# Performance work log

Hardware: AMD Instinct MI355X
Metric: run time of the kernel (lower is better)

Reference implementation:

```python
import jax, jax.numpy as jnp
import numpy as np

NUM_EXPERTS = 8
HIDDEN = 2048
FFN = 1376
CAPACITY_FACTOR = 1.25
SCORE_SCALE = 1.0


def setup_inputs() -> dict:
    key = jax.random.key(0)
    k = jax.random.split(key, 6)
    T = 8192
    x = jax.random.normal(k[0], (T, HIDDEN), dtype=jnp.float32)
    topK_indices = jax.random.randint(k[1], (T,), 0, NUM_EXPERTS, dtype=jnp.int64)
    topK_scores = jax.random.uniform(k[2], (T,), dtype=jnp.float32)
    s = 1.0 / np.sqrt(HIDDEN)
    w_gate = jax.random.normal(k[3], (NUM_EXPERTS, HIDDEN, FFN), dtype=jnp.float32) * s
    w_up = jax.random.normal(k[4], (NUM_EXPERTS, HIDDEN, FFN), dtype=jnp.float32) * s
    w_down = jax.random.normal(k[5], (NUM_EXPERTS, FFN, HIDDEN), dtype=jnp.float32) * (1.0 / np.sqrt(FFN))
    return {"x": x, "topK_indices": topK_indices, "topK_scores": topK_scores,
            "w_gate": w_gate, "w_up": w_up, "w_down": w_down}


def reference(x, topK_indices, topK_scores, w_gate, w_up, w_down):
    T, D = x.shape
    E = w_gate.shape[0]
    capacity = int(CAPACITY_FACTOR * T / E)  # static (depends only on shapes)
    # position of each token within its assigned expert (deterministic drop:
    # keep the first `capacity` tokens in sequence order per expert)
    oh = jax.nn.one_hot(topK_indices, E, dtype=jnp.int32)          # [T,E]
    rank = jnp.take_along_axis(jnp.cumsum(oh, axis=0) - 1,
                               topK_indices[:, None].astype(jnp.int32), axis=1)[:, 0]
    keep = rank < capacity                                          # [T]
    # dispatch into per-expert capacity buffers; dropped tokens go to dummy slot
    slot = jnp.where(keep, topK_indices.astype(jnp.int32) * capacity + rank, E * capacity)
    buf = jnp.zeros((E * capacity + 1, D), x.dtype)
    buf = buf.at[slot].set(jnp.where(keep[:, None], x, jnp.zeros_like(x)))
    xe = buf[:E * capacity].reshape(E, capacity, D)                 # [E,C,D]
    # per-expert SwiGLU MLP as grouped GEMMs
    h = jax.nn.silu(jnp.einsum('ecd,edf->ecf', xe, w_gate)) * jnp.einsum('ecd,edf->ecf', xe, w_up)
    out = jnp.einsum('ecf,efd->ecd', h, w_down).reshape(E * capacity, D)
    out = jnp.concatenate([out, jnp.zeros((1, D), out.dtype)], axis=0)
    # combine: dropped tokens -> zero (dropped_padding='zero'), gate-score fusion
    y = out[slot] * keep[:, None].astype(out.dtype)
    y = y * (topK_scores[:, None] * SCORE_SCALE)
    return y
```

## Files before the change

kernel.cpp:

```cpp
#include <hip/hip_runtime.h>
#include <hip/hip_bf16.h>
#include <cstdint>
#include <cstddef>

#define NTOK 8192
#define DH   2048
#define DF   1376
#define NE   8
#define CAP  1280

typedef __bf16 bf16x8 __attribute__((ext_vector_type(8)));
typedef float  f32x4  __attribute__((ext_vector_type(4)));

#define BARRIER() asm volatile("s_barrier" ::: "memory")
#define WAITV(n)  asm volatile("s_waitcnt vmcnt(" #n ")" ::: "memory")
#define LGKM0()   asm volatile("s_waitcnt lgkmcnt(0)" ::: "memory")
#define SCHED0()  __builtin_amdgcn_sched_barrier(0)
#define SETPRIO(n) __builtin_amdgcn_s_setprio(n)

__device__ __forceinline__ uint32_t pk2(float a, float b) {
  float2 f; f.x = a; f.y = b;
  union { __hip_bfloat162 h; uint32_t u; } cv;
  cv.h = __float22bfloat162_rn(f);
  return cv.u;
}
__device__ __forceinline__ ushort bf16bits(float a) {
  return (ushort)(pk2(a, 0.f) & 0xFFFFu);
}
__device__ __forceinline__ void gload16(const ushort* g, ushort* l) {
  __builtin_amdgcn_global_load_lds(
      (const __attribute__((address_space(1))) uint32_t*)(const void*)g,
      (__attribute__((address_space(3))) uint32_t*)(void*)l,
      16, 0, 0);
}

__device__ __forceinline__ void rp_src(int o, int& row, int& ko) {
  int p = o >> 7;
  int g = ((o >> 4) & 7) ^ (p & 7);
  row = p * 2 + (g >> 2);
  ko  = (g & 3) * 8;
}
__device__ __forceinline__ int rp_off(int row, int l4) {
  return ((row >> 1) << 7) + (((((row & 1) << 2) + l4) ^ ((row >> 1) & 7)) << 4);
}

__global__ void routing_kernel(const int* __restrict__ idx, int* __restrict__ tok_slot,
                               int* __restrict__ tok_keep) {
  __shared__ int cnt[256][NE];
  const int t = threadIdx.x;
  for (int s = t; s < NE * CAP; s += 256) tok_slot[s] = -1;
  unsigned long long cA = 0ull, cB = 0ull;
  const int per = NTOK / 256, base = t * per;
  for (int i = 0; i < per; ++i) {
    int e = idx[base + i];
    unsigned long long inc = 1ull << ((e & 3) * 16);
    if (e < 4) cA += inc; else cB += inc;
  }
#pragma unroll
  for (int e = 0; e < 4; ++e) cnt[t][e]     = (int)((cA >> (e * 16)) & 0xFFFF);
#pragma unroll
  for (int e = 0; e < 4; ++e) cnt[t][4 + e] = (int)((cB >> (e * 16)) & 0xFFFF);
  __syncthreads();
  if (t < NE) {
    int run = 0;
    for (int i = 0; i < 256; ++i) { int c = cnt[i][t]; cnt[i][t] = run; run += c; }
  }
  __syncthreads();
  cA = 0ull; cB = 0ull;
#pragma unroll
  for (int e = 0; e < 4; ++e) cA |= (unsigned long long)(cnt[t][e] & 0xFFFF) << (e * 16);
#pragma unroll
  for (int e = 0; e < 4; ++e) cB |= (unsigned long long)(cnt[t][4 + e] & 0xFFFF) << (e * 16);
  for (int i = 0; i < per; ++i) {
    int token = base + i;
    int e = idx[token];
    int sh = (e & 3) * 16;
    int r = (int)(((e < 4 ? cA : cB) >> sh) & 0xFFFF);
    unsigned long long inc = 1ull << sh;
    if (e < 4) cA += inc; else cB += inc;
    bool keep = (r < CAP);
    tok_keep[token] = keep ? 1 : 0;
    if (keep) tok_slot[e * CAP + r] = token;
  }
}

__global__ void xconv_zero(const float* __restrict__ x, const int* __restrict__ keep,
                           ushort* __restrict__ xb, float* __restrict__ y) {
  const int row = blockIdx.x;
  const int c = threadIdx.x * 8;
  const size_t off = (size_t)row * DH + c;
  float4 a = *(const float4*)(x + off);
  float4 b = *(const float4*)(x + off + 4);
  uint4 p = { pk2(a.x, a.y), pk2(a.z, a.w), pk2(b.x, b.y), pk2(b.z, b.w) };
  *(uint4*)(xb + off) = p;
  if (!keep[row]) {
    float4 z = {0.f, 0.f, 0.f, 0.f};
    *(float4*)(y + off) = z;
    *(float4*)(y + off + 4) = z;
  }
}

__global__ __launch_bounds__(256) void transpose_all(
    const float* __restrict__ wg, const float* __restrict__ wu, const float* __restrict__ wd,
    ushort* __restrict__ wgt, ushort* __restrict__ wut, ushort* __restrict__ wdt) {
  const int z = blockIdx.z;
  const float* in; ushort* out; int K, N, eidx;
  if (z < 8)       { in = wg; out = wgt; K = DH; N = DF; eidx = z; }
  else if (z < 16) { in = wu; out = wut; K = DH; N = DF; eidx = z - 8; }
  else             { in = wd; out = wdt; K = DF; N = DH; eidx = z - 16; }
  const int n0 = blockIdx.x * 64, k0 = blockIdx.y * 64;
  if (n0 >= N || k0 >= K) return;
  __shared__ ushort T[64][72];
  const int tid = threadIdx.x;
  const size_t eoff_in  = (size_t)eidx * K * N;
  const size_t eoff_out = (size_t)eidx * N * K;
  const int kr = tid >> 4;
  const int nc = (tid & 15) * 4;
#pragma unroll
  for (int it = 0; it < 4; ++it) {
    int k = k0 + kr + it * 16;
    int n = n0 + nc;
    float4 v = {0.f, 0.f, 0.f, 0.f};
    if (k < K && n + 4 <= N) v = *(const float4*)(in + eoff_in + (size_t)k * N + n);
    T[nc + 0][kr + it * 16] = bf16bits(v.x);
    T[nc + 1][kr + it * 16] = bf16bits(v.y);
    T[nc + 2][kr + it * 16] = bf16bits(v.z);
    T[nc + 3][kr + it * 16] = bf16bits(v.w);
  }
  __syncthreads();
  const int nr = tid >> 2;
  const int kc = tid & 3;
#pragma unroll
  for (int it = 0; it < 2; ++it) {
    int kloc = kc * 16 + it * 8;
    int n = n0 + nr, k = k0 + kloc;
    if (n < N && k + 8 <= K)
      *(uint4*)(out + eoff_out + (size_t)n * K + k) = *(const uint4*)&T[nr][kloc];
  }
}

__global__ __launch_bounds__(512, 4) void gemm_gateup4(
    const ushort* __restrict__ xb, const ushort* __restrict__ wgt,
    const ushort* __restrict__ wut, const int* __restrict__ tok_slot,
    ushort* __restrict__ h)
{
  __shared__ __align__(16) char sm[73728];
  const int tid = threadIdx.x, lane = tid & 63, wid = tid >> 6;
  const int wr = wid >> 1, wc = wid & 1;
  const int l15 = lane & 15, l4 = lane >> 4;

  int wgid = (blockIdx.x & 7) * 110 + (blockIdx.x >> 3);
  const int e = wgid / 110;
  const int rem = wgid - e * 110;
  const int mt = rem % 10, nt = rem / 10;
  const int n0 = nt * 128;

  const ushort* srcA; const ushort* srcBg; const ushort* srcBu;
  {
    int o = wid * 1024 + lane * 16;
    int row, ko; rp_src(o, row, ko);
    int tk = tok_slot[e * CAP + mt * 128 + row];
    if (tk < 0) tk = 0;
    srcA = xb + (size_t)tk * DH + ko;
    int n = n0 + row; if (n > DF - 1) n = DF - 1;
    srcBg = wgt + ((size_t)e * DF + n) * DH + ko;
    srcBu = wut + ((size_t)e * DF + n) * DH + ko;
  }
  int aoff[2], boff[4];
#pragma unroll
  for (int i = 0; i < 2; ++i) aoff[i] = rp_off(wr * 32 + i * 16 + l15, l4);
#pragma unroll
  for (int j = 0; j < 4; ++j) boff[j] = rp_off(wc * 64 + j * 16 + l15, l4);
  const int dstw = wid * 1024;

  f32x4 accG[2][4], accU[2][4];
#pragma unroll
  for (int i = 0; i < 2; ++i)
#pragma unroll
    for (int j = 0; j < 4; ++j) {
      accG[i][j] = (f32x4){0.f, 0.f, 0.f, 0.f};
      accU[i][j] = (f32x4){0.f, 0.f, 0.f, 0.f};
    }

  const int NT = DH / 32;
#pragma unroll
  for (int t0 = 0; t0 < 2; ++t0) {
    int kk = t0 * 32;
    gload16(srcA  + kk, (ushort*)(sm + t0 * 8192 + dstw));
    gload16(srcBg + kk, (ushort*)(sm + 24576 + t0 * 8192 + dstw));
    gload16(srcBu + kk, (ushort*)(sm + 49152 + t0 * 8192 + dstw));
  }
  WAITV(3);
  BARRIER();

  int rb = 0, wb = 2;
  for (int t = 0; t < NT; ++t) {
    char* Ab  = sm + rb * 8192;
    char* Bgb = sm + 24576 + rb * 8192;
    char* Bub = sm + 49152 + rb * 8192;
    if (t + 2 < NT) {
      const int kk = (t + 2) * 32;
      gload16(srcA  + kk, (ushort*)(sm + wb * 8192 + dstw));
      gload16(srcBg + kk, (ushort*)(sm + 24576 + wb * 8192 + dstw));
      gload16(srcBu + kk, (ushort*)(sm + 49152 + wb * 8192 + dstw));
    }
    bf16x8 a[2], b[4];
#pragma unroll
    for (int i = 0; i < 2; ++i) a[i] = *(const bf16x8*)(Ab + aoff[i]);
#pragma unroll
    for (int j = 0; j < 4; ++j) b[j] = *(const bf16x8*)(Bgb + boff[j]);
    LGKM0(); SCHED0();
    SETPRIO(1);
#pragma unroll
    for (int j = 0; j < 4; ++j)
#pragma unroll
      for (int i = 0; i < 2; ++i)
        accG[i][j] = __builtin_amdgcn_mfma_f32_16x16x32_bf16(a[i], b[j], accG[i][j], 0, 0, 0);
    SETPRIO(0); SCHED0();
#pragma unroll
    for (int j = 0; j < 4; ++j) b[j] = *(const bf16x8*)(Bub + boff[j]);
    LGKM0(); SCHED0();
    SETPRIO(1);
#pragma unroll
    for (int j = 0; j < 4; ++j)
#pragma unroll
      for (int i = 0; i < 2; ++i)
        accU[i][j] = __builtin_amdgcn_mfma_f32_16x16x32_bf16(a[i], b[j], accU[i][j], 0, 0, 0);
    SETPRIO(0); SCHED0();
    if (t + 2 < NT) { WAITV(3); } else { WAITV(0); }
    BARRIER();
    rb = (rb == 2) ? 0 : rb + 1;
    wb = (wb == 2) ? 0 : wb + 1;
  }
  const size_t rowbase = (size_t)(e * CAP + mt * 128 + wr * 32);
#pragma unroll
  for (int j = 0; j < 4; ++j) {
    int col = n0 + wc * 64 + j * 16 + l15;
    if (col < DF) {
#pragma unroll
      for (int i = 0; i < 2; ++i)
#pragma unroll
        for (int r2 = 0; r2 < 4; ++r2) {
          size_t row = rowbase + i * 16 + l4 * 4 + r2;
          float gv = accG[i][j][r2], uv = accU[i][j][r2];
          h[row * DF + col] = bf16bits(gv / (1.f + __expf(-gv)) * uv);
        }
    }
  }
}

__global__ __launch_bounds__(512, 4) void gemm_down4(
    const ushort* __restrict__ h, const ushort* __restrict__ wdt,
    const int* __restrict__ tok_slot, const float* __restrict__ scores,
    float* __restrict__ y)
{
  __shared__ __align__(16) char sm[50176];
  int* tokc = (int*)(sm + 49152);
  float* scc = (float*)(sm + 49664);
  const int tid = threadIdx.x, lane = tid & 63, wid = tid >> 6;
  const int wr = wid >> 1, wc = wid & 1;
  const int l15 = lane & 15, l4 = lane >> 4;

  int wgid = (blockIdx.x & 7) * 160 + (blockIdx.x >> 3);
  const int e = wgid / 160;
  const int rem = wgid - e * 160;
  const int mt = rem % 10, nt = rem / 10;
  const int n0 = nt * 128;

  if (tid < 128) {
    int tk = tok_slot[e * CAP + mt * 128 + tid];
    tokc[tid] = tk;
    scc[tid] = (tk >= 0) ? scores[tk] : 0.f;
  }
  __syncthreads();

  const size_t hrow0 = (size_t)(e * CAP + mt * 128);
  const ushort* srcA; const ushort* srcB;
  {
    int o = wid * 1024 + lane * 16;
    int row, ko; rp_src(o, row, ko);
    srcA = h + (hrow0 + row) * DF + ko;
    srcB = wdt + ((size_t)e * DH + n0 + row) * DF + ko;
  }
  int aoff[2], boff[4];
#pragma unroll
  for (int i = 0; i < 2; ++i) aoff[i] = rp_off(wr * 32 + i * 16 + l15, l4);
#pragma unroll
  for (int j = 0; j < 4; ++j) boff[j] = rp_off(wc * 64 + j * 16 + l15, l4);
  const int dstw = wid * 1024;

  f32x4 acc[2][4];
#pragma unroll
  for (int i = 0; i < 2; ++i)
#pragma unroll
    for (int j = 0; j < 4; ++j) acc[i][j] = (f32x4){0.f, 0.f, 0.f, 0.f};

  const int NT = DF / 32;
#pragma unroll
  for (int t0 = 0; t0 < 2; ++t0) {
    int kk = t0 * 32;
    gload16(srcA + kk, (ushort*)(sm + t0 * 8192 + dstw));
    gload16(srcB + kk, (ushort*)(sm + 24576 + t0 * 8192 + dstw));
  }
  WAITV(2);
  BARRIER();

  int rb = 0, wb = 2;
  for (int t = 0; t < NT; ++t) {
    char* Ab = sm + rb * 8192;
    char* Bb = sm + 24576 + rb * 8192;
    if (t + 2 < NT) {
      const int kk = (t + 2) * 32;
      gload16(srcA + kk, (ushort*)(sm + wb * 8192 + dstw));
      gload16(srcB + kk, (ushort*)(sm + 24576 + wb * 8192 + dstw));
    }
    bf16x8 a[2], b[4];
#pragma unroll
    for (int i = 0; i < 2; ++i) a[i] = *(const bf16x8*)(Ab + aoff[i]);
#pragma unroll
    for (int j = 0; j < 4; ++j) b[j] = *(const bf16x8*)(Bb + boff[j]);
    LGKM0(); SCHED0();
    SETPRIO(1);
#pragma unroll
    for (int j = 0; j < 4; ++j)
#pragma unroll
      for (int i = 0; i < 2; ++i)
        acc[i][j] = __builtin_amdgcn_mfma_f32_16x16x32_bf16(a[i], b[j], acc[i][j], 0, 0, 0);
    SETPRIO(0); SCHED0();
    if (t + 2 < NT) { WAITV(2); } else { WAITV(0); }
    BARRIER();
    rb = (rb == 2) ? 0 : rb + 1;
    wb = (wb == 2) ? 0 : wb + 1;
  }
  int tkr[2][4]; float sr[2][4];
#pragma unroll
  for (int i = 0; i < 2; ++i)
#pragma unroll
    for (int r = 0; r < 4; ++r) {
      int rl = wr * 32 + i * 16 + l4 * 4 + r;
      tkr[i][r] = tokc[rl];
      sr[i][r]  = scc[rl];
    }
#pragma unroll
  for (int j = 0; j < 4; ++j) {
    int col = n0 + wc * 64 + j * 16 + l15;
#pragma unroll
    for (int i = 0; i < 2; ++i)
#pragma unroll
      for (int r = 0; r < 4; ++r)
        if (tkr[i][r] >= 0)
          y[(size_t)tkr[i][r] * DH + col] = acc[i][j][r] * sr[i][r];
  }
}

extern "C" void kernel_launch(void* const* d_in, const int* in_sizes, int n_in,
                              void* d_out, int out_size, void* d_ws, size_t ws_size,
                              hipStream_t stream) {
  const float* x   = (const float*)d_in[0];
  const int*   idx = (const int*)d_in[1];
  const float* sc  = (const float*)d_in[2];
  const float* wg  = (const float*)d_in[3];
  const float* wu  = (const float*)d_in[4];
  const float* wd  = (const float*)d_in[5];
  float* y = (float*)d_out;

  const size_t OFF_KEEP = 40960;
  const size_t OFF_H    = 73728;
  const size_t SZ_H     = (size_t)NE * CAP * DF * 2;
  const size_t OFF_XB   = OFF_H + SZ_H;
  const size_t SZ_XB    = (size_t)NTOK * DH * 2;
  const size_t OFF_WGT  = OFF_XB + SZ_XB;
  const size_t SZ_W     = (size_t)NE * DH * DF * 2;
  const size_t OFF_WUT  = OFF_WGT + SZ_W;
  const size_t OFF_WDT  = OFF_WUT + SZ_W;

  int* tok_slot = (int*)d_ws;
  int* tok_keep = (int*)((char*)d_ws + OFF_KEEP);
  ushort* hbuf = (ushort*)((char*)d_ws + OFF_H);
  ushort* xb   = (ushort*)((char*)d_ws + OFF_XB);
  ushort* wgt  = (ushort*)((char*)d_ws + OFF_WGT);
  ushort* wut  = (ushort*)((char*)d_ws + OFF_WUT);
  ushort* wdt  = (ushort*)((char*)d_ws + OFF_WDT);

  hipLaunchKernelGGL(routing_kernel, dim3(1), dim3(256), 0, stream, idx, tok_slot, tok_keep);
  hipLaunchKernelGGL(xconv_zero, dim3(NTOK), dim3(256), 0, stream, x, tok_keep, xb, y);
  hipLaunchKernelGGL(transpose_all, dim3(32, 32, 24), dim3(256), 0, stream,
                     wg, wu, wd, wgt, wut, wdt);
  hipLaunchKernelGGL(gemm_gateup4, dim3(880), dim3(512), 0, stream,
                     xb, wgt, wut, tok_slot, hbuf);
  hipLaunchKernelGGL(gemm_down4, dim3(1280), dim3(512), 0, stream,
                     hbuf, wdt, tok_slot, sc, y);
}
```

Baseline: 347.1 us.

## Make grouped GEMM kernels persistent with atomic tile counter scheduling

Both expert GEMM kernels become persistent: a fixed grid of 512 workgroups repeatedly claims tile indices from a global atomic counter until all tiles are done. The routing kernel zeroes the two counters. The aim is to remove wave-quantization tail effects and per-block launch overhead by matching the grid to resident capacity. In exchange it adds a per-tile atomic and barrier, and it drops the earlier XCD-aware mapping of blocks to experts, which may reduce L2 locality for the weights.

Result: slower. 388.5 us (+11.9%).

```diff
diff --git a/kernel.cpp b/kernel.cpp
--- a/kernel.cpp
+++ b/kernel.cpp
@@ -9,6 +9,9 @@
 #define NE   8
 #define CAP  1280
 
+#define GU_NTILES 880
+#define DN_NTILES 1280
+
 typedef __bf16 bf16x8 __attribute__((ext_vector_type(8)));
 typedef float  f32x4  __attribute__((ext_vector_type(4)));
 
@@ -45,9 +48,10 @@
 }
 
 __global__ void routing_kernel(const int* __restrict__ idx, int* __restrict__ tok_slot,
-                               int* __restrict__ tok_keep) {
+                               int* __restrict__ tok_keep, int* __restrict__ ctrs) {
   __shared__ int cnt[256][NE];
   const int t = threadIdx.x;
+  if (t < 2) ctrs[t] = 0;
   for (int s = t; s < NE * CAP; s += 256) tok_slot[s] = -1;
   unsigned long long cA = 0ull, cB = 0ull;
   const int per = NTOK / 256, base = t * per;
@@ -139,33 +143,17 @@
   }
 }
 
-__global__ __launch_bounds__(512, 4) void gemm_gateup4(
+__global__ __launch_bounds__(512, 4) void gemm_gateup6(
     const ushort* __restrict__ xb, const ushort* __restrict__ wgt,
     const ushort* __restrict__ wut, const int* __restrict__ tok_slot,
-    ushort* __restrict__ h)
+    ushort* __restrict__ h, int* __restrict__ ctr)
 {
   __shared__ __align__(16) char sm[73728];
+  __shared__ int tile_s;
   const int tid = threadIdx.x, lane = tid & 63, wid = tid >> 6;
   const int wr = wid >> 1, wc = wid & 1;
   const int l15 = lane & 15, l4 = lane >> 4;
 
-  int wgid = (blockIdx.x & 7) * 110 + (blockIdx.x >> 3);
-  const int e = wgid / 110;
-  const int rem = wgid - e * 110;
-  const int mt = rem % 10, nt = rem / 10;
-  const int n0 = nt * 128;
-
-  const ushort* srcA; const ushort* srcBg; const ushort* srcBu;
-  {
-    int o = wid * 1024 + lane * 16;
-    int row, ko; rp_src(o, row, ko);
-    int tk = tok_slot[e * CAP + mt * 128 + row];
-    if (tk < 0) tk = 0;
-    srcA = xb + (size_t)tk * DH + ko;
-    int n = n0 + row; if (n > DF - 1) n = DF - 1;
-    srcBg = wgt + ((size_t)e * DF + n) * DH + ko;
-    srcBu = wut + ((size_t)e * DF + n) * DH + ko;
-  }
   int aoff[2], boff[4];
 #pragma unroll
   for (int i = 0; i < 2; ++i) aoff[i] = rp_off(wr * 32 + i * 16 + l15, l4);
@@ -173,115 +161,119 @@
   for (int j = 0; j < 4; ++j) boff[j] = rp_off(wc * 64 + j * 16 + l15, l4);
   const int dstw = wid * 1024;
 
-  f32x4 accG[2][4], accU[2][4];
-#pragma unroll
-  for (int i = 0; i < 2; ++i)
+  int srow, sko;
+  { int o = wid * 1024 + lane * 16; rp_src(o, srow, sko); }
+
+  for (;;) {
+    if (tid == 0) tile_s = atomicAdd(ctr, 1);
+    __syncthreads();
+    const int tile = tile_s;
+    if (tile >= GU_NTILES) break;
+    const int e = tile / 110;
+    const int rem = tile - e * 110;
+    const int nt = rem / 10, mt = rem - (rem / 10) * 10;
+    const int n0 = nt * 128;
+
+    const ushort* srcA; const ushort* srcBg; const ushort* srcBu;
+    {
+      int tk = tok_slot[e * CAP + mt * 128 + srow];
+      if (tk < 0) tk = 0;
+      srcA = xb + (size_t)tk * DH + sko;
+      int n = n0 + srow; if (n > DF - 1) n = DF - 1;
+      srcBg = wgt + ((size_t)e * DF + n) * DH + sko;
+      srcBu = wut + ((size_t)e * DF + n) * DH + sko;
+    }
+
+    f32x4 accG[2][4], accU[2][4];
+#pragma unroll
+    for (int i = 0; i < 2; ++i)
+#pragma unroll
+      for (int j = 0; j < 4; ++j) {
+        accG[i][j] = (f32x4){0.f, 0.f, 0.f, 0.f};
+        accU[i][j] = (f32x4){0.f, 0.f, 0.f, 0.f};
+      }
+
+    const int NT = DH / 32;
+#pragma unroll
+    for (int t0 = 0; t0 < 2; ++t0) {
+      int kk = t0 * 32;
+      gload16(srcA  + kk, (ushort*)(sm + t0 * 8192 + dstw));
+      gload16(srcBg + kk, (ushort*)(sm + 24576 + t0 * 8192 + dstw));
+      gload16(srcBu + kk, (ushort*)(sm + 49152 + t0 * 8192 + dstw));
+    }
+    WAITV(3);
+    BARRIER();
+
+    int rb = 0, wb = 2;
+    for (int t = 0; t < NT; ++t) {
+      char* Ab  = sm + rb * 8192;
+      char* Bgb = sm + 24576 + rb * 8192;
+      char* Bub = sm + 49152 + rb * 8192;
+      if (t + 2 < NT) {
+        const int kk = (t + 2) * 32;
+        gload16(srcA  + kk, (ushort*)(sm + wb * 8192 + dstw));
+        gload16(srcBg + kk, (ushort*)(sm + 24576 + wb * 8192 + dstw));
+        gload16(srcBu + kk, (ushort*)(sm + 49152 + wb * 8192 + dstw));
+      }
+      bf16x8 a[2], b[4];
+#pragma unroll
+      for (int i = 0; i < 2; ++i) a[i] = *(const bf16x8*)(Ab + aoff[i]);
+#pragma unroll
+      for (int j = 0; j < 4; ++j) b[j] = *(const bf16x8*)(Bgb + boff[j]);
+      LGKM0(); SCHED0();
+      SETPRIO(1);
+#pragma unroll
+      for (int j = 0; j < 4; ++j)
+#pragma unroll
+        for (int i = 0; i < 2; ++i)
+          accG[i][j] = __builtin_amdgcn_mfma_f32_16x16x32_bf16(a[i], b[j], accG[i][j], 0, 0, 0);
+      SETPRIO(0); SCHED0();
+#pragma unroll
+      for (int j = 0; j < 4; ++j) b[j] = *(const bf16x8*)(Bub + boff[j]);
+      LGKM0(); SCHED0();
+      SETPRIO(1);
+#pragma unroll
+      for (int j = 0; j < 4; ++j)
+#pragma unroll
+        for (int i = 0; i < 2; ++i)
+          accU[i][j] = __builtin_amdgcn_mfma_f32_16x16x32_bf16(a[i], b[j], accU[i][j], 0, 0, 0);
+      SETPRIO(0); SCHED0();
+      if (t + 2 < NT) { WAITV(3); } else { WAITV(0); }
+      BARRIER();
+      rb = (rb == 2) ? 0 : rb + 1;
+      wb = (wb == 2) ? 0 : wb + 1;
+    }
+    const size_t rowbase = (size_t)(e * CAP + mt * 128 + wr * 32);
 #pragma unroll
     for (int j = 0; j < 4; ++j) {
-      accG[i][j] = (f32x4){0.f, 0.f, 0.f, 0.f};
-      accU[i][j] = (f32x4){0.f, 0.f, 0.f, 0.f};
-    }
-
-  const int NT = DH / 32;
-#pragma unroll
-  for (int t0 = 0; t0 < 2; ++t0) {
-    int kk = t0 * 32;
-    gload16(srcA  + kk, (ushort*)(sm + t0 * 8192 + dstw));
-    gload16(srcBg + kk, (ushort*)(sm + 24576 + t0 * 8192 + dstw));
-    gload16(srcBu + kk, (ushort*)(sm + 49152 + t0 * 8192 + dstw));
-  }
-  WAITV(3);
-  BARRIER();
-
-  int rb = 0, wb = 2;
-  for (int t = 0; t < NT; ++t) {
-    char* Ab  = sm + rb * 8192;
-    char* Bgb = sm + 24576 + rb * 8192;
-    char* Bub = sm + 49152 + rb * 8192;
-    if (t + 2 < NT) {
-      const int kk = (t + 2) * 32;
-      gload16(srcA  + kk, (ushort*)(sm + wb * 8192 + dstw));
-      gload16(srcBg + kk, (ushort*)(sm + 24576 + wb * 8192 + dstw));
-      gload16(srcBu + kk, (ushort*)(sm + 49152 + wb * 8192 + dstw));
-    }
-    bf16x8 a[2], b[4];
-#pragma unroll
-    for (int i = 0; i < 2; ++i) a[i] = *(const bf16x8*)(Ab + aoff[i]);
-#pragma unroll
-    for (int j = 0; j < 4; ++j) b[j] = *(const bf16x8*)(Bgb + boff[j]);
-    LGKM0(); SCHED0();
-    SETPRIO(1);
-#pragma unroll
-    for (int j = 0; j < 4; ++j)
-#pragma unroll
-      for (int i = 0; i < 2; ++i)
-        accG[i][j] = __builtin_amdgcn_mfma_f32_16x16x32_bf16(a[i], b[j], accG[i][j], 0, 0, 0);
-    SETPRIO(0); SCHED0();
-#pragma unroll
-    for (int j = 0; j < 4; ++j) b[j] = *(const bf16x8*)(Bub + boff[j]);
-    LGKM0(); SCHED0();
-    SETPRIO(1);
-#pragma unroll
-    for (int j = 0; j < 4; ++j)
-#pragma unroll
-      for (int i = 0; i < 2; ++i)
-        accU[i][j] = __builtin_amdgcn_mfma_f32_16x16x32_bf16(a[i], b[j], accU[i][j], 0, 0, 0);
-    SETPRIO(0); SCHED0();
-    if (t + 2 < NT) { WAITV(3); } else { WAITV(0); }
-    BARRIER();
-    rb = (rb == 2) ? 0 : rb + 1;
-    wb = (wb == 2) ? 0 : wb + 1;
-  }
-  const size_t rowbase = (size_t)(e * CAP + mt * 128 + wr * 32);
-#pragma unroll
-  for (int j = 0; j < 4; ++j) {
-    int col = n0 + wc * 64 + j * 16 + l15;
-    if (col < DF) {
-#pragma unroll
-      for (int i = 0; i < 2; ++i)
-#pragma unroll
-        for (int r2 = 0; r2 < 4; ++r2) {
-          size_t row = rowbase + i * 16 + l4 * 4 + r2;
-          float gv = accG[i][j][r2], uv = accU[i][j][r2];
-          h[row * DF + col] = bf16bits(gv / (1.f + __expf(-gv)) * uv);
-        }
-    }
-  }
-}
-
-__global__ __launch_bounds__(512, 4) void gemm_down4(
+      int col = n0 + wc * 64 + j * 16 + l15;
+      if (col < DF) {
+#pragma unroll
+        for (int i = 0; i < 2; ++i)
+#pragma unroll
+          for (int r2 = 0; r2 < 4; ++r2) {
+            size_t row = rowbase + i * 16 + l4 * 4 + r2;
+            float gv = accG[i][j][r2], uv = accU[i][j][r2];
+            h[row * DF + col] = bf16bits(gv / (1.f + __expf(-gv)) * uv);
+          }
+      }
+    }
+  }
+}
+
+__global__ __launch_bounds__(512, 4) void gemm_down6(
     const ushort* __restrict__ h, const ushort* __restrict__ wdt,
     const int* __restrict__ tok_slot, const float* __restrict__ scores,
-    float* __restrict__ y)
+    float* __restrict__ y, int* __restrict__ ctr)
 {
   __shared__ __align__(16) char sm[50176];
+  __shared__ int tile_s;
   int* tokc = (int*)(sm + 49152);
   float* scc = (float*)(sm + 49664);
   const int tid = threadIdx.x, lane = tid & 63, wid = tid >> 6;
   const int wr = wid >> 1, wc = wid & 1;
   const int l15 = lane & 15, l4 = lane >> 4;
 
-  int wgid = (blockIdx.x & 7) * 160 + (blockIdx.x >> 3);
-  const int e = wgid / 160;
-  const int rem = wgid - e * 160;
-  const int mt = rem % 10, nt = rem / 10;
-  const int n0 = nt * 128;
-
-  if (tid < 128) {
-    int tk = tok_slot[e * CAP + mt * 128 + tid];
-    tokc[tid] = tk;
-    scc[tid] = (tk >= 0) ? scores[tk] : 0.f;
-  }
-  __syncthreads();
-
-  const size_t hrow0 = (size_t)(e * CAP + mt * 128);
-  const ushort* srcA; const ushort* srcB;
-  {
-    int o = wid * 1024 + lane * 16;
-    int row, ko; rp_src(o, row, ko);
-    srcA = h + (hrow0 + row) * DF + ko;
-    srcB = wdt + ((size_t)e * DH + n0 + row) * DF + ko;
-  }
   int aoff[2], boff[4];
 #pragma unroll
   for (int i = 0; i < 2; ++i) aoff[i] = rp_off(wr * 32 + i * 16 + l15, l4);
@@ -289,67 +281,86 @@
   for (int j = 0; j < 4; ++j) boff[j] = rp_off(wc * 64 + j * 16 + l15, l4);
   const int dstw = wid * 1024;
 
-  f32x4 acc[2][4];
-#pragma unroll
-  for (int i = 0; i < 2; ++i)
-#pragma unroll
-    for (int j = 0; j < 4; ++j) acc[i][j] = (f32x4){0.f, 0.f, 0.f, 0.f};
-
-  const int NT = DF / 32;
-#pragma unroll
-  for (int t0 = 0; t0 < 2; ++t0) {
-    int kk = t0 * 32;
-    gload16(srcA + kk, (ushort*)(sm + t0 * 8192 + dstw));
-    gload16(srcB + kk, (ushort*)(sm + 24576 + t0 * 8192 + dstw));
-  }
-  WAITV(2);
-  BARRIER();
-
-  int rb = 0, wb = 2;
-  for (int t = 0; t < NT; ++t) {
-    char* Ab = sm + rb * 8192;
-    char* Bb = sm + 24576 + rb * 8192;
-    if (t + 2 < NT) {
-      const int kk = (t + 2) * 32;
-      gload16(srcA + kk, (ushort*)(sm + wb * 8192 + dstw));
-      gload16(srcB + kk, (ushort*)(sm + 24576 + wb * 8192 + dstw));
-    }
-    bf16x8 a[2], b[4];
-#pragma unroll
-    for (int i = 0; i < 2; ++i) a[i] = *(const bf16x8*)(Ab + aoff[i]);
-#pragma unroll
-    for (int j = 0; j < 4; ++j) b[j] = *(const bf16x8*)(Bb + boff[j]);
-    LGKM0(); SCHED0();
-    SETPRIO(1);
-#pragma unroll
-    for (int j = 0; j < 4; ++j)
+  int srow, sko;
+  { int o = wid * 1024 + lane * 16; rp_src(o, srow, sko); }
+
+  for (;;) {
+    if (tid == 0) tile_s = atomicAdd(ctr, 1);
+    __syncthreads();
+    const int tile = tile_s;
+    if (tile >= DN_NTILES) break;
+    const int e = tile / 160;
+    const int rem = tile - e * 160;
+    const int nt = rem / 10, mt = rem - (rem / 10) * 10;
+    const int n0 = nt * 128;
+
+    if (tid < 128) {
+      int tk = tok_slot[e * CAP + mt * 128 + tid];
+      tokc[tid] = tk;
+      scc[tid] = (tk >= 0) ? scores[tk] : 0.f;
+    }
+    __syncthreads();
+
+    const size_t hrow0 = (size_t)(e * CAP + mt * 128);
+    const ushort* srcA = h + (hrow0 + srow) * DF + sko;
+    const ushort* srcB = wdt + ((size_t)e * DH + n0 + srow) * DF + sko;
+
+    f32x4 acc[2][4];
+#pragma unroll
+    for (int i = 0; i < 2; ++i)
+#pragma unroll
+      for (int j = 0; j < 4; ++j) acc[i][j] = (f32x4){0.f, 0.f, 0.f, 0.f};
+
+    const int NT = DF / 32;
+#pragma unroll
+    for (int t0 = 0; t0 < 2; ++t0) {
+      int kk = t0 * 32;
+      gload16(srcA + kk, (ushort*)(sm + t0 * 8192 + dstw));
+      gload16(srcB + kk, (ushort*)(sm + 24576 + t0 * 8192 + dstw));
+    }
+    WAITV(2);
+    BARRIER();
+
+    int rb = 0, wb = 2;
+    for (int t = 0; t < NT; ++t) {
+      char* Ab = sm + rb * 8192;
+      char* Bb = sm + 24576 + rb * 8192;
+      if (t + 2 < NT) {
+        const int kk = (t + 2) * 32;
+        gload16(srcA + kk, (ushort*)(sm + wb * 8192 + dstw));
+        gload16(srcB + kk, (ushort*)(sm + 24576 + wb * 8192 + dstw));
+      }
+      bf16x8 a[2], b[4];
+#pragma unroll
+      for (int i = 0; i < 2; ++i) a[i] = *(const bf16x8*)(Ab + aoff[i]);
+#pragma unroll
+      for (int j = 0; j < 4; ++j) b[j] = *(const bf16x8*)(Bb + boff[j]);
+      LGKM0(); SCHED0();
+      SETPRIO(1);
+#pragma unroll
+      for (int j = 0; j < 4; ++j)
+#pragma unroll
+        for (int i = 0; i < 2; ++i)
+          acc[i][j] = __builtin_amdgcn_mfma_f32_16x16x32_bf16(a[i], b[j], acc[i][j], 0, 0, 0);
+      SETPRIO(0); SCHED0();
+      if (t + 2 < NT) { WAITV(2); } else { WAITV(0); }
+      BARRIER();
+      rb = (rb == 2) ? 0 : rb + 1;
+      wb = (wb == 2) ? 0 : wb + 1;
+    }
+#pragma unroll
+    for (int j = 0; j < 4; ++j) {
+      int col = n0 + wc * 64 + j * 16 + l15;
 #pragma unroll
       for (int i = 0; i < 2; ++i)
-        acc[i][j] = __builtin_amdgcn_mfma_f32_16x16x32_bf16(a[i], b[j], acc[i][j], 0, 0, 0);
-    SETPRIO(0); SCHED0();
-    if (t + 2 < NT) { WAITV(2); } else { WAITV(0); }
-    BARRIER();
-    rb = (rb == 2) ? 0 : rb + 1;
-    wb = (wb == 2) ? 0 : wb + 1;
-  }
-  int tkr[2][4]; float sr[2][4];
-#pragma unroll
-  for (int i = 0; i < 2; ++i)
-#pragma unroll
-    for (int r = 0; r < 4; ++r) {
-      int rl = wr * 32 + i * 16 + l4 * 4 + r;
-      tkr[i][r] = tokc[rl];
-      sr[i][r]  = scc[rl];
-    }
-#pragma unroll
-  for (int j = 0; j < 4; ++j) {
-    int col = n0 + wc * 64 + j * 16 + l15;
-#pragma unroll
-    for (int i = 0; i < 2; ++i)
-#pragma unroll
-      for (int r = 0; r < 4; ++r)
-        if (tkr[i][r] >= 0)
-          y[(size_t)tkr[i][r] * DH + col] = acc[i][j][r] * sr[i][r];
+#pragma unroll
+        for (int r = 0; r < 4; ++r) {
+          int rl = wr * 32 + i * 16 + l4 * 4 + r;
+          int tk = tokc[rl];
+          if (tk >= 0)
+            y[(size_t)tk * DH + col] = acc[i][j][r] * scc[rl];
+        }
+    }
   }
 }
 
@@ -365,7 +376,8 @@
   float* y = (float*)d_out;
 
   const size_t OFF_KEEP = 40960;
-  const size_t OFF_H    = 73728;
+  const size_t OFF_CTR  = OFF_KEEP + NTOK * 4;
+  const size_t OFF_H    = 77824;
   const size_t SZ_H     = (size_t)NE * CAP * DF * 2;
   const size_t OFF_XB   = OFF_H + SZ_H;
   const size_t SZ_XB    = (size_t)NTOK * DH * 2;
@@ -376,18 +388,19 @@
 
   int* tok_slot = (int*)d_ws;
   int* tok_keep = (int*)((char*)d_ws + OFF_KEEP);
+  int* ctrs     = (int*)((char*)d_ws + OFF_CTR);
   ushort* hbuf = (ushort*)((char*)d_ws + OFF_H);
   ushort* xb   = (ushort*)((char*)d_ws + OFF_XB);
   ushort* wgt  = (ushort*)((char*)d_ws + OFF_WGT);
   ushort* wut  = (ushort*)((char*)d_ws + OFF_WUT);
   ushort* wdt  = (ushort*)((char*)d_ws + OFF_WDT);
 
-  hipLaunchKernelGGL(routing_kernel, dim3(1), dim3(256), 0, stream, idx, tok_slot, tok_keep);
+  hipLaunchKernelGGL(routing_kernel, dim3(1), dim3(256), 0, stream, idx, tok_slot, tok_keep, ctrs);
   hipLaunchKernelGGL(xconv_zero, dim3(NTOK), dim3(256), 0, stream, x, tok_keep, xb, y);
   hipLaunchKernelGGL(transpose_all, dim3(32, 32, 24), dim3(256), 0, stream,
                      wg, wu, wd, wgt, wut, wdt);
-  hipLaunchKernelGGL(gemm_gateup4, dim3(880), dim3(512), 0, stream,
-                     xb, wgt, wut, tok_slot, hbuf);
-  hipLaunchKernelGGL(gemm_down4, dim3(1280), dim3(512), 0, stream,
-                     hbuf, wdt, tok_slot, sc, y);
-}
+  hipLaunchKernelGGL(gemm_gateup6, dim3(512), dim3(512), 0, stream,
+                     xb, wgt, wut, tok_slot, hbuf, ctrs + 0);
+  hipLaunchKernelGGL(gemm_down6, dim3(512), dim3(512), 0, stream,
+                     hbuf, wdt, tok_slot, sc, y, ctrs + 1);
+}
```
